# Performance work log

Hardware: AMD Instinct MI355X
Metric: run time of the kernel (lower is better)

Reference implementation:

```python
import jax, jax.numpy as jnp
import numpy as np

H = 16
HD = 128
ROPE_BASE = 10000.0

def _rope_cos_sin(T, dtype):
    inv_freq = 1.0 / (ROPE_BASE ** (jnp.arange(0, HD, 2, dtype=jnp.float32) / HD))  # [HD/2]
    pos = jnp.arange(T, dtype=jnp.float32)
    freqs = pos[:, None] * inv_freq[None, :]  # [T, HD/2]
    return jnp.cos(freqs).astype(dtype), jnp.sin(freqs).astype(dtype)

def _apply_rotary(x, cos, sin):
    # x: [B,H,T,HD]; cos/sin: [T,HD/2]
    x1, x2 = x[..., : HD // 2], x[..., HD // 2 :]
    c = cos[None, None, :, :]
    s = sin[None, None, :, :]
    return jnp.concatenate([x1 * c - x2 * s, x1 * s + x2 * c], axis=-1)

def setup_inputs() -> dict:
    key = jax.random.key(0)
    ks = jax.random.split(key, 5)
    B, T, D = 2, 2048, 2048
    x = jax.random.normal(ks[0], (B, T, D), dtype=jnp.float32)
    Wqkv = jax.random.normal(ks[1], (3 * D, D), dtype=jnp.float32) * (D ** -0.5)
    bqkv = jax.random.normal(ks[2], (3 * D,), dtype=jnp.float32) * 0.02
    Wo = jax.random.normal(ks[3], (D, D), dtype=jnp.float32) * (D ** -0.5)
    bo = jax.random.normal(ks[4], (D,), dtype=jnp.float32) * 0.02
    # causal mask: True = masked (future positions)
    mask = jnp.triu(jnp.ones((T, T), dtype=bool), k=1)[None, None, :, :]
    return {"x": x, "Wqkv": Wqkv, "bqkv": bqkv, "Wo": Wo, "bo": bo, "mask": mask}

def reference(x, Wqkv, bqkv, Wo, bo, mask):
    B, T, D = x.shape
    qkv = x @ Wqkv.T + bqkv  # [B,T,3D]
    q, k, v = jnp.split(qkv, 3, axis=-1)
    def to_heads(t):
        return t.reshape(B, T, H, HD).transpose(0, 2, 1, 3)  # [B,H,T,HD]
    q, k, v = to_heads(q), to_heads(k), to_heads(v)
    cos, sin = _rope_cos_sin(T, x.dtype)
    q = _apply_rotary(q, cos, sin)
    k = _apply_rotary(k, cos, sin)
    scale = HD ** 0.5
    attn = jnp.einsum('bhqd,bhkd->bhqk', q, k) / scale
    neg = -jnp.finfo(x.dtype).max
    attn = jnp.where(mask, neg, attn)
    w = jax.nn.softmax(attn, axis=-1)
    out = jnp.einsum('bhqk,bhkd->bhqd', w, v)  # [B,H,T,HD]
    out = out.transpose(0, 2, 1, 3).reshape(B, T, H * HD)
    return out @ Wo.T + bo
```

## Files before the change

### kernel.cpp

```cpp
#include <hip/hip_runtime.h>
#include <hip/hip_bf16.h>
#include <cstdint>

typedef __bf16 bf16;
typedef __bf16 bf16x8 __attribute__((ext_vector_type(8)));
typedef float  f32x4  __attribute__((ext_vector_type(4)));

#define B_   2
#define T_   2048
#define D_   2048
#define H_   16
#define HD_  128

typedef __attribute__((address_space(3))) void       lds_void;
typedef __attribute__((address_space(1))) const void gbl_void;
__device__ __forceinline__ void glds16(const bf16* g, bf16* l) {
    __builtin_amdgcn_global_load_lds((gbl_void*)g, (lds_void*)l, 16, 0, 0);
}

__device__ __forceinline__ ushort4 cvt4(const float4 v) {
    union { bf16 h[4]; ushort4 u; } pk;
    pk.h[0] = (bf16)v.x; pk.h[1] = (bf16)v.y;
    pk.h[2] = (bf16)v.z; pk.h[3] = (bf16)v.w;
    return pk.u;
}

__global__ __launch_bounds__(256) void convert_xw_kernel(
    const float* __restrict__ x, const float* __restrict__ wqkv,
    bf16* __restrict__ xb, bf16* __restrict__ wqkvb)
{
    const int NX = (B_ * T_ * D_) / 4;
    const int NT = NX + (3 * D_ * D_) / 4;
    for (int g = blockIdx.x * blockDim.x + threadIdx.x; g < NT;
         g += gridDim.x * blockDim.x) {
        if (g < NX) ((ushort4*)xb)[g]      = cvt4(((const float4*)x)[g]);
        else        ((ushort4*)wqkvb)[g-NX] = cvt4(((const float4*)wqkv)[g-NX]);
    }
}

__global__ __launch_bounds__(256) void convert_wo_kernel(
    const float* __restrict__ wo, bf16* __restrict__ wob)
{
    const int N = (D_ * D_) / 4;
    for (int g = blockIdx.x * blockDim.x + threadIdx.x; g < N;
         g += gridDim.x * blockDim.x)
        ((ushort4*)wob)[g] = cvt4(((const float4*)wo)[g]);
}

__device__ __forceinline__ void gemm_core_glds(
    const bf16* __restrict__ A, const bf16* __restrict__ W, int K,
    int bm, int bn, int tid, f32x4 (&acc)[4][4],
    bf16* lds_a, bf16* lds_b)
{
    const int lane = tid & 63, quad = lane >> 4, lcol = lane & 15;
    const int wave = tid >> 6;
    const int wm = (wave >> 1) * 64, wn2 = (wave & 1) * 32;
    const int sw = lcol & 7;
    const int sr = tid >> 3, pc = tid & 7;
    const int sc = (pc ^ (sr & 7)) * 8;
    const bf16* abase = A + (size_t)(bm * 128 + sr) * K + sc;
    const bf16* bbase = W + (size_t)(bn * 128 + sr) * K + sc;
    bf16* la = lds_a + sr * 64 + pc * 8;
    bf16* lb = lds_b + sr * 64 + pc * 8;

    for (int k0 = 0; k0 < K; k0 += 64) {
        __syncthreads();
#pragma unroll
        for (int p = 0; p < 4; p++) {
            glds16(abase + k0 + (size_t)32 * p * K, la + 2048 * p);
            glds16(bbase + k0 + (size_t)32 * p * K, lb + 2048 * p);
        }
        __syncthreads();
#pragma unroll
        for (int kk = 0; kk < 2; kk++) {
            bf16x8 af[4], bfr[4];
#pragma unroll
            for (int i = 0; i < 4; i++)
                af[i] = *(const bf16x8*)&lds_a[(wm + i * 16 + lcol) * 64 +
                                               (((kk * 4 + quad) ^ sw) * 8)];
#pragma unroll
            for (int j = 0; j < 4; j++) {
                const int row = wn2 + (j & 1) * 16 + (j >> 1) * 64 + lcol;
                bfr[j] = *(const bf16x8*)&lds_b[row * 64 +
                                                (((kk * 4 + quad) ^ sw) * 8)];
            }
#pragma unroll
            for (int i = 0; i < 4; i++)
#pragma unroll
                for (int j = 0; j < 4; j++)
                    acc[i][j] = __builtin_amdgcn_mfma_f32_16x16x32_bf16(af[i], bfr[j], acc[i][j], 0, 0, 0);
        }
    }
}

__global__ __launch_bounds__(256) void qkv_gemm_kernel(
    const bf16* __restrict__ xb, const bf16* __restrict__ wqkvb,
    const float* __restrict__ bias,
    bf16* __restrict__ qh, bf16* __restrict__ kh, bf16* __restrict__ vT)
{
    __shared__ bf16 lds_a[128 * 64];
    __shared__ bf16 lds_b[128 * 64];
    const int tid = threadIdx.x;
    const int bm = blockIdx.y, bn = blockIdx.x;
    const int lane = tid & 63, quad = lane >> 4, lcol = lane & 15;
    const int wave = tid >> 6;
    const int wm = (wave >> 1) * 64, wn2 = (wave & 1) * 32;

    f32x4 acc[4][4];
    const f32x4 z = {0.f, 0.f, 0.f, 0.f};
#pragma unroll
    for (int i = 0; i < 4; i++)
#pragma unroll
        for (int j = 0; j < 4; j++) acc[i][j] = z;

    gemm_core_glds(xb, wqkvb, D_, bm, bn, tid, acc, lds_a, lds_b);

    const int n0 = bn * 128;
    const int part = bn / 16;
    const int h = bn & 15;
    const int mb0 = bm * 128 + wm;

    if (part < 2) {
        bf16* dst = (part == 0) ? qh : kh;
#pragma unroll
        for (int i = 0; i < 4; i++) {
#pragma unroll
            for (int jp = 0; jp < 2; jp++) {
                const int d1 = wn2 + jp * 16 + lcol;
                const float invf = __expf(-0.14391156831212787f * (float)d1);
                const float b1 = bias[n0 + d1];
                const float b2 = bias[n0 + d1 + 64];
#pragma unroll
                for (int r = 0; r < 4; r++) {
                    const int m = mb0 + i * 16 + quad * 4 + r;
                    const int bb = m >> 11, t = m & (T_ - 1);
                    const float x1 = acc[i][jp][r] + b1;
                    const float x2 = acc[i][jp + 2][r] + b2;
                    float s, c;
                    __sincosf((float)t * invf, &s, &c);
                    const size_t rowo = ((size_t)(bb * H_ + h) * T_ + t) * HD_;
                    dst[rowo + d1]      = (bf16)(x1 * c - x2 * s);
                    dst[rowo + d1 + 64] = (bf16)(x1 * s + x2 * c);
                }
            }
        }
    } else {
        const int bb = mb0 >> 11, t64 = mb0 & (T_ - 1);
        const int bh = bb * H_ + h;
#pragma unroll
        for (int j = 0; j < 4; j++) {
            const int d = wn2 + (j & 1) * 16 + (j >> 1) * 64 + lcol;
            const float bv = bias[n0 + d];
            bf16* vdst = &vT[((size_t)bh * HD_ + d) * T_ + t64];
#pragma unroll
            for (int r = 0; r < 4; r++) {
                union { bf16 hh[4]; ushort4 u; } pk;
#pragma unroll
                for (int i = 0; i < 4; i++) pk.hh[i] = (bf16)(acc[i][j][r] + bv);
                *(ushort4*)&vdst[(quad * 4 + r) * 4] = pk.u;
            }
        }
    }
}

__global__ __launch_bounds__(256) void attn_kernel(
    const bf16* __restrict__ qh, const bf16* __restrict__ kh,
    const bf16* __restrict__ vT, bf16* __restrict__ ctx)
{
    __shared__ bf16 lds_k[2][64 * 128];
    __shared__ bf16 lds_v[2][128 * 64];
    __shared__ bf16 lds_p[64 * 64];
    const int tid = threadIdx.x;
    const int id = blockIdx.x;
    const int bh = id & 31;
    const int qt = 31 - ((id >> 5) & 31);
    const int q0 = qt * 64;
    const int lane = tid & 63, quad = lane >> 4, lcol = lane & 15;
    const int wave = tid >> 6;
    const int wq0 = wave * 16;
    const float scale2 = 0.08838834764831845f * 1.4426950408889634f;

    const bf16* kbase = kh + (size_t)bh * T_ * HD_;
    const bf16* vbase = vT + (size_t)bh * HD_ * T_;

    const int ksrow = tid >> 4;
    const bf16* kstage = kbase + (size_t)ksrow * HD_ + (((tid & 15) ^ ksrow) << 3);
    const int vsd = tid >> 3;
    const bf16* vstage = vbase + (size_t)vsd * T_ + (((tid & 7) ^ (vsd & 7)) << 3);

    bf16x8 qf[4];
#pragma unroll
    for (int kk = 0; kk < 4; kk++)
        qf[kk] = *(const bf16x8*)&qh[((size_t)bh * T_ + q0 + wq0 + lcol) * HD_ +
                                     kk * 32 + quad * 8];

    f32x4 o[8];
    const f32x4 z = {0.f, 0.f, 0.f, 0.f};
#pragma unroll
    for (int jd = 0; jd < 8; jd++) o[jd] = z;
    float l_part[4] = {0.f, 0.f, 0.f, 0.f};

    const int ktmax = qt + 1;
#pragma unroll
    for (int p = 0; p < 4; p++) {
        glds16(kstage + (size_t)16 * p * HD_, &lds_k[0][tid * 8 + p * 2048]);
        glds16(vstage + (size_t)32 * p * T_, &lds_v[0][tid * 8 + p * 2048]);
    }

    for (int kt = 0; kt < ktmax; kt++) {
        __syncthreads();
        if (kt + 1 < ktmax) {
            const bf16* ks = kstage + (size_t)(kt + 1) * 64 * HD_;
            const bf16* vs = vstage + (kt + 1) * 64;
            bf16* lkd = &lds_k[(kt + 1) & 1][tid * 8];
            bf16* lvd = &lds_v[(kt + 1) & 1][tid * 8];
#pragma unroll
            for (int p = 0; p < 4; p++) {
                glds16(ks + (size_t)16 * p * HD_, lkd + p * 2048);
                glds16(vs + (size_t)32 * p * T_, lvd + p * 2048);
            }
        }
        const bf16* lk = lds_k[kt & 1];
        const bf16* lv = lds_v[kt & 1];

        f32x4 s_acc[4];
#pragma unroll
        for (int j = 0; j < 4; j++) s_acc[j] = z;
        __builtin_amdgcn_s_setprio(1);
#pragma unroll
        for (int kk = 0; kk < 4; kk++) {
#pragma unroll
            for (int j = 0; j < 4; j++) {
                const bf16x8 bk = *(const bf16x8*)&lk[(j * 16 + lcol) * 128 +
                                        (((kk * 4 + quad) ^ lcol) << 3)];
                s_acc[j] = __builtin_amdgcn_mfma_f32_16x16x32_bf16(qf[kk], bk, s_acc[j], 0, 0, 0);
            }
        }
        __builtin_amdgcn_s_setprio(0);

        const bool diag = (kt == qt);
#pragma unroll
        for (int r = 0; r < 4; r++) {
            const int prow = wq0 + quad * 4 + r;
            const int qrow = q0 + prow;
            union { bf16 hh[4]; ushort4 u; } pk;
            float lp = 0.f;
#pragma unroll
            for (int j = 0; j < 4; j++) {
                float p = exp2f(fmaf(s_acc[j][r], scale2, -16.0f));
                if (diag) {
                    const int kcol = kt * 64 + j * 16 + lcol;
                    p = (kcol > qrow) ? 0.f : p;
                }
                lp += p;
                pk.hh[j] = (bf16)p;
            }
            l_part[r] += lp;
            *(ushort4*)&lds_p[prow * 64 + ((lcol * 4) ^ ((prow & 7) << 3))] = pk.u;
        }

#pragma unroll
        for (int kk2 = 0; kk2 < 2; kk2++) {
            const int prow = wq0 + lcol;
            const bf16x8 pf = *(const bf16x8*)&lds_p[prow * 64 +
                                  ((kk2 * 32 + quad * 8) ^ ((lcol & 7) << 3))];
            bf16x8 vf[8];
#pragma unroll
            for (int jd = 0; jd < 8; jd++) {
                const int d = jd * 16 + lcol;
                vf[jd] = *(const bf16x8*)&lv[d * 64 +
                              (((kk2 * 4 + quad) ^ (lcol & 7)) << 3)];
            }
            __builtin_amdgcn_s_setprio(1);
#pragma unroll
            for (int jd = 0; jd < 8; jd++)
                o[jd] = __builtin_amdgcn_mfma_f32_16x16x32_bf16(pf, vf[jd], o[jd], 0, 0, 0);
            __builtin_amdgcn_s_setprio(0);
        }
    }

    float inv_l[4];
#pragma unroll
    for (int r = 0; r < 4; r++) {
        float rs = l_part[r];
#pragma unroll
        for (int off = 1; off < 16; off <<= 1)
            rs += __shfl_xor(rs, off);
        inv_l[r] = 1.0f / rs;
    }
    const int b = bh >> 4, h = bh & 15;
#pragma unroll
    for (int r = 0; r < 4; r++) {
        const int t = q0 + wq0 + quad * 4 + r;
#pragma unroll
        for (int jd = 0; jd < 8; jd++)
            ctx[((size_t)(b * T_ + t)) * D_ + h * HD_ + jd * 16 + lcol] =
                (bf16)(o[jd][r] * inv_l[r]);
    }
}

__global__ __launch_bounds__(256) void proj_gemm_kernel(
    const bf16* __restrict__ ctx, const bf16* __restrict__ wob,
    const float* __restrict__ bias, float* __restrict__ out)
{
    __shared__ bf16 lds_a[128 * 64];
    __shared__ bf16 lds_b[128 * 64];
    const int tid = threadIdx.x;
    const int bm = blockIdx.y, bn = blockIdx.x;
    const int lane = tid & 63, quad = lane >> 4, lcol = lane & 15;
    const int wave = tid >> 6;
    const int wm = (wave >> 1) * 64, wn2 = (wave & 1) * 32;

    f32x4 acc[4][4];
    const f32x4 z = {0.f, 0.f, 0.f, 0.f};
#pragma unroll
    for (int i = 0; i < 4; i++)
#pragma unroll
        for (int j = 0; j < 4; j++) acc[i][j] = z;

    gemm_core_glds(ctx, wob, D_, bm, bn, tid, acc, lds_a, lds_b);

    const int n0 = bn * 128;
#pragma unroll
    for (int i = 0; i < 4; i++) {
#pragma unroll
        for (int j = 0; j < 4; j++) {
            const int n = n0 + wn2 + (j & 1) * 16 + (j >> 1) * 64 + lcol;
            const float bv = bias[n];
#pragma unroll
            for (int r = 0; r < 4; r++) {
                const int m = bm * 128 + wm + i * 16 + quad * 4 + r;
                out[(size_t)m * D_ + n] = acc[i][j][r] + bv;
            }
        }
    }
}

extern "C" void kernel_launch(void* const* d_in, const int* in_sizes, int n_in,
                              void* d_out, int out_size, void* d_ws, size_t ws_size,
                              hipStream_t stream)
{
    const float* x    = (const float*)d_in[0];
    const float* Wqkv = (const float*)d_in[1];
    const float* bqkv = (const float*)d_in[2];
    const float* Wo   = (const float*)d_in[3];
    const float* bo   = (const float*)d_in[4];
    float* out = (float*)d_out;

    const size_t HT = (size_t)B_ * H_ * T_ * HD_;
    bf16* xb   = (bf16*)d_ws;
    bf16* qh   = xb + HT;
    bf16* kh   = qh + HT;
    bf16* vT   = kh + HT;
    bf16* ctx  = xb;
    bf16* wob  = qh;
    bf16* wqkvb = (bf16*)d_out;

    convert_xw_kernel<<<2560, 256, 0, stream>>>(x, Wqkv, xb, wqkvb);
    qkv_gemm_kernel<<<dim3(48, 32), 256, 0, stream>>>(xb, wqkvb, bqkv, qh, kh, vT);
    attn_kernel<<<1024, 256, 0, stream>>>(qh, kh, vT, ctx);
    convert_wo_kernel<<<1024, 256, 0, stream>>>(Wo, wob);
    proj_gemm_kernel<<<dim3(16, 32), 256, 0, stream>>>(ctx, wob, bo, out);
}
```

Measured before the change: 365.2 us.

## Pair causal query tiles per block to balance attention work

Each attention block now handles two query tiles, qtA = 31-qp and qtB = qp, and runs a fixed 33 key-tile iterations, with an epilogue and Q reload between the two tiles. The grid is halved from 1024 to 512 blocks. This removes the triangular load imbalance of causal attention, where blocks with late query tiles take far longer than early ones and leave a long tail. In exchange each block runs longer and the grid is smaller, so there is less parallelism to hide latency on a large GPU, and the mid-loop epilogue adds a stall.

```diff
diff --git a/kernel.cpp b/kernel.cpp
--- a/kernel.cpp
+++ b/kernel.cpp
@@ -173,12 +173,15 @@
     const int tid = threadIdx.x;
     const int id = blockIdx.x;
     const int bh = id & 31;
-    const int qt = 31 - ((id >> 5) & 31);
-    const int q0 = qt * 64;
+    const int qp = id >> 5;
+    const int qtA = 31 - qp;
+    const int qtB = qp;
+    const int ktA = qtA + 1;
     const int lane = tid & 63, quad = lane >> 4, lcol = lane & 15;
     const int wave = tid >> 6;
     const int wq0 = wave * 16;
     const float scale2 = 0.08838834764831845f * 1.4426950408889634f;
+    const int b = bh >> 4, h = bh & 15;
 
     const bf16* kbase = kh + (size_t)bh * T_ * HD_;
     const bf16* vbase = vT + (size_t)bh * HD_ * T_;
@@ -188,11 +191,17 @@
     const int vsd = tid >> 3;
     const bf16* vstage = vbase + (size_t)vsd * T_ + (((tid & 7) ^ (vsd & 7)) << 3);
 
+    int qt_cur = qtA;
+    int q0 = qtA * 64;
+
     bf16x8 qf[4];
-#pragma unroll
-    for (int kk = 0; kk < 4; kk++)
-        qf[kk] = *(const bf16x8*)&qh[((size_t)bh * T_ + q0 + wq0 + lcol) * HD_ +
-                                     kk * 32 + quad * 8];
+    auto load_q = [&](int q0_) {
+#pragma unroll
+        for (int kk = 0; kk < 4; kk++)
+            qf[kk] = *(const bf16x8*)&qh[((size_t)bh * T_ + q0_ + wq0 + lcol) * HD_ +
+                                         kk * 32 + quad * 8];
+    };
+    load_q(q0);
 
     f32x4 o[8];
     const f32x4 z = {0.f, 0.f, 0.f, 0.f};
@@ -200,28 +209,59 @@
     for (int jd = 0; jd < 8; jd++) o[jd] = z;
     float l_part[4] = {0.f, 0.f, 0.f, 0.f};
 
-    const int ktmax = qt + 1;
+    auto do_epilogue = [&](int q0_) {
+        float inv_l[4];
+#pragma unroll
+        for (int r = 0; r < 4; r++) {
+            float rs = l_part[r];
+#pragma unroll
+            for (int off = 1; off < 16; off <<= 1)
+                rs += __shfl_xor(rs, off);
+            inv_l[r] = 1.0f / rs;
+        }
+#pragma unroll
+        for (int r = 0; r < 4; r++) {
+            const int t = q0_ + wq0 + quad * 4 + r;
+#pragma unroll
+            for (int jd = 0; jd < 8; jd++)
+                ctx[((size_t)(b * T_ + t)) * D_ + h * HD_ + jd * 16 + lcol] =
+                    (bf16)(o[jd][r] * inv_l[r]);
+        }
+    };
+
 #pragma unroll
     for (int p = 0; p < 4; p++) {
         glds16(kstage + (size_t)16 * p * HD_, &lds_k[0][tid * 8 + p * 2048]);
         glds16(vstage + (size_t)32 * p * T_, &lds_v[0][tid * 8 + p * 2048]);
     }
 
-    for (int kt = 0; kt < ktmax; kt++) {
+    for (int s = 0; s < 33; s++) {
         __syncthreads();
-        if (kt + 1 < ktmax) {
-            const bf16* ks = kstage + (size_t)(kt + 1) * 64 * HD_;
-            const bf16* vs = vstage + (kt + 1) * 64;
-            bf16* lkd = &lds_k[(kt + 1) & 1][tid * 8];
-            bf16* lvd = &lds_v[(kt + 1) & 1][tid * 8];
+        if (s + 1 < 33) {
+            const int kn = (s + 1 < ktA) ? (s + 1) : (s + 1 - ktA);
+            const bf16* ks = kstage + (size_t)kn * 64 * HD_;
+            const bf16* vs = vstage + kn * 64;
+            bf16* lkd = &lds_k[(s + 1) & 1][tid * 8];
+            bf16* lvd = &lds_v[(s + 1) & 1][tid * 8];
 #pragma unroll
             for (int p = 0; p < 4; p++) {
                 glds16(ks + (size_t)16 * p * HD_, lkd + p * 2048);
                 glds16(vs + (size_t)32 * p * T_, lvd + p * 2048);
             }
         }
-        const bf16* lk = lds_k[kt & 1];
-        const bf16* lv = lds_v[kt & 1];
+        if (s == ktA) {
+            do_epilogue(q0);
+            qt_cur = qtB;
+            q0 = qtB * 64;
+            load_q(q0);
+#pragma unroll
+            for (int jd = 0; jd < 8; jd++) o[jd] = z;
+#pragma unroll
+            for (int r = 0; r < 4; r++) l_part[r] = 0.f;
+        }
+        const int kt = (s < ktA) ? s : (s - ktA);
+        const bf16* lk = lds_k[s & 1];
+        const bf16* lv = lds_v[s & 1];
 
         f32x4 s_acc[4];
 #pragma unroll
@@ -238,7 +278,7 @@
         }
         __builtin_amdgcn_s_setprio(0);
 
-        const bool diag = (kt == qt);
+        const bool diag = (kt == qt_cur);
 #pragma unroll
         for (int r = 0; r < 4; r++) {
             const int prow = wq0 + quad * 4 + r;
@@ -279,24 +319,7 @@
         }
     }
 
-    float inv_l[4];
-#pragma unroll
-    for (int r = 0; r < 4; r++) {
-        float rs = l_part[r];
-#pragma unroll
-        for (int off = 1; off < 16; off <<= 1)
-            rs += __shfl_xor(rs, off);
-        inv_l[r] = 1.0f / rs;
-    }
-    const int b = bh >> 4, h = bh & 15;
-#pragma unroll
-    for (int r = 0; r < 4; r++) {
-        const int t = q0 + wq0 + quad * 4 + r;
-#pragma unroll
-        for (int jd = 0; jd < 8; jd++)
-            ctx[((size_t)(b * T_ + t)) * D_ + h * HD_ + jd * 16 + lcol] =
-                (bf16)(o[jd][r] * inv_l[r]);
-    }
+    do_epilogue(q0);
 }
 
 __global__ __launch_bounds__(256) void proj_gemm_kernel(
@@ -358,7 +381,7 @@
 
     convert_xw_kernel<<<2560, 256, 0, stream>>>(x, Wqkv, xb, wqkvb);
     qkv_gemm_kernel<<<dim3(48, 32), 256, 0, stream>>>(xb, wqkvb, bqkv, qh, kh, vT);
-    attn_kernel<<<1024, 256, 0, stream>>>(qh, kh, vT, ctx);
+    attn_kernel<<<512, 256, 0, stream>>>(qh, kh, vT, ctx);
     convert_wo_kernel<<<1024, 256, 0, stream>>>(Wo, wob);
     proj_gemm_kernel<<<dim3(16, 32), 256, 0, stream>>>(ctx, wob, bo, out);
 }
```

After: 354.6 us. 2.9% less time.
